# Kernel optimization log

Measured on AMD Instinct MI355X. Metric: run time of the kernel, lower is better.

## Reference

```python
import jax, jax.numpy as jnp
import numpy as np

N_HEAD = 16
THETA = 10000.0


def _rope_cos_sin(T, head_dim):
    # freqs: (T, head_dim//2), matches torch.polar(ones, outer(t, 1/theta^(2i/d)))
    inv = 1.0 / (THETA ** (jnp.arange(0, head_dim, 2, dtype=jnp.float32) / head_dim))
    freqs = jnp.arange(T, dtype=jnp.float32)[:, None] * inv[None, :]
    # broadcast shape (1, T, 1, head_dim//2) over (B, T, H, head_dim//2)
    return jnp.cos(freqs)[None, :, None, :], jnp.sin(freqs)[None, :, None, :]


def _apply_rope(t, cos, sin):
    # t: (B, T, H, hd); pairs (even, odd) form complex numbers
    B, T, H, hd = t.shape
    tr = t.astype(jnp.float32).reshape(B, T, H, hd // 2, 2)
    re, im = tr[..., 0], tr[..., 1]
    out = jnp.stack([re * cos - im * sin, re * sin + im * cos], axis=-1)
    return out.reshape(B, T, H, hd).astype(t.dtype)


def setup_inputs() -> dict:
    key = jax.random.key(0)
    k1, k2, k3 = jax.random.split(key, 3)
    C = 1024
    x = jax.random.normal(k1, (4, 2048, C), dtype=jnp.float32)
    w_attn = jax.random.normal(k2, (3 * C, C), dtype=jnp.float32) * 0.02
    w_proj = jax.random.normal(k3, (C, C), dtype=jnp.float32) * 0.02
    return {"x": x, "w_attn": w_attn, "w_proj": w_proj}


def reference(x, w_attn, w_proj):
    B, T, C = x.shape
    H = N_HEAD
    hd = C // H
    qkv = x @ w_attn.T  # (B, T, 3C) fused QKV projection
    q, k, v = jnp.split(qkv, 3, axis=-1)
    q = q.reshape(B, T, H, hd)
    k = k.reshape(B, T, H, hd)
    v = v.reshape(B, T, H, hd).transpose(0, 2, 1, 3)  # (B, H, T, hd)
    cos, sin = _rope_cos_sin(T, hd)
    q = _apply_rope(q, cos, sin).transpose(0, 2, 1, 3)  # (B, H, T, hd)
    k = _apply_rope(k, cos, sin).transpose(0, 2, 1, 3)
    scale = 1.0 / jnp.sqrt(jnp.float32(hd))
    scores = jnp.einsum('bhqd,bhkd->bhqk', q, k) * scale
    attn = jax.nn.softmax(scores, axis=-1)
    y = jnp.einsum('bhqk,bhkd->bhqd', attn, v)  # (B, H, T, hd)
    y = y.transpose(0, 2, 1, 3).reshape(B, T, C)
    return y @ w_proj.T
```

## Files before the change

### kernel.cpp

```cpp
#include <hip/hip_runtime.h>
#include <math.h>

#define BATCH 4
#define TSEQ 2048
#define CDIM 1024
#define NHEAD 16
#define HDIM 64
#define M_ROWS (BATCH * TSEQ)

typedef float f32x4 __attribute__((ext_vector_type(4)));
typedef __bf16 bf16x8 __attribute__((ext_vector_type(8)));
typedef unsigned int u32x4 __attribute__((ext_vector_type(4)));

typedef const __attribute__((address_space(1))) void gas_void;
typedef __attribute__((address_space(3))) void las_void;

static __device__ __forceinline__ unsigned short f2bf(float f) {
    unsigned int x = __float_as_uint(f);
    x += 0x7fffu + ((x >> 16) & 1u);
    return (unsigned short)(x >> 16);
}

__global__ void prep_kernel(const float* __restrict__ x, unsigned short* __restrict__ xb,
                            const float* __restrict__ wa, unsigned short* __restrict__ wab,
                            const float* __restrict__ wp, unsigned short* __restrict__ wpb,
                            float* __restrict__ cosT, float* __restrict__ sinT) {
    int blk = blockIdx.x;
    if (blk < 6144) {
        const float* in;
        unsigned short* out;
        int base;
        if (blk < 4096)      { in = x;  out = xb;  base = blk; }
        else if (blk < 5632) { in = wa; out = wab; base = blk - 4096; }
        else                 { in = wp; out = wpb; base = blk - 5632; }
        int i = (base * 256 + threadIdx.x) << 3;
        float4 a = *(const float4*)(in + i);
        float4 b = *(const float4*)(in + i + 4);
        union { unsigned short u[8]; u32x4 v; } pk;
        pk.u[0] = f2bf(a.x); pk.u[1] = f2bf(a.y); pk.u[2] = f2bf(a.z); pk.u[3] = f2bf(a.w);
        pk.u[4] = f2bf(b.x); pk.u[5] = f2bf(b.y); pk.u[6] = f2bf(b.z); pk.u[7] = f2bf(b.w);
        *(u32x4*)(out + i) = pk.v;
    } else {
        int idx = (blk - 6144) * 256 + threadIdx.x;
        int t = idx >> 5;
        int i = idx & 31;
        double inv = pow(10000.0, -((double)(2 * i)) / (double)HDIM);
        double ph = (double)t * inv;
        cosT[idx] = (float)cos(ph);
        sinT[idx] = (float)sin(ph);
    }
}

#define GROW(p) (((p) & 64) + (((p) & 15) << 2) + (((p) >> 4) & 3))
#define GEMM_CORE(A_, B_, K_, bm_, bn_)                                          \
    const int tid = threadIdx.x;                                                 \
    const int w = tid >> 6, lane = tid & 63;                                     \
    const int l15 = lane & 15, quad = lane >> 4;                                 \
    const int wm = w >> 1, wn = w & 1;                                           \
    const int ksw = ((lane & 7) ^ ((lane >> 3) & 7)) << 3;                       \
    const int rx = l15 & 7;                                                      \
    const unsigned short* Ag[4]; const unsigned short* Bg[4];                    \
    unsigned short* Al[4]; unsigned short* Bl[4];                                \
    _Pragma("unroll")                                                            \
    for (int i = 0; i < 4; ++i) {                                                \
        const int row = (w << 5) + (i << 3) + (lane >> 3);                       \
        Ag[i] = A_ + (size_t)(bm_ + row) * K_ + ksw;                             \
        Bg[i] = B_ + (size_t)(bn_ + GROW(row)) * K_ + ksw;                       \
        Al[i] = As + row * 64 + ((lane & 7) << 3);                               \
        Bl[i] = Bs + row * 64 + ((lane & 7) << 3);                               \
    }                                                                            \
    f32x4 acc[4][4];                                                             \
    _Pragma("unroll")                                                            \
    for (int i = 0; i < 4; ++i)                                                  \
        _Pragma("unroll")                                                        \
        for (int j = 0; j < 4; ++j) acc[i][j] = (f32x4){0.f, 0.f, 0.f, 0.f};     \
    _Pragma("unroll")                                                            \
    for (int t = 0; t < K_ / 64; ++t) {                                          \
        _Pragma("unroll")                                                        \
        for (int i = 0; i < 4; ++i) {                                            \
            __builtin_amdgcn_global_load_lds((gas_void*)(Ag[i] + t * 64), (las_void*)Al[i], 16, 0, 0); \
            __builtin_amdgcn_global_load_lds((gas_void*)(Bg[i] + t * 64), (las_void*)Bl[i], 16, 0, 0); \
        }                                                                        \
        __syncthreads();                                                         \
        _Pragma("unroll")                                                        \
        for (int kk = 0; kk < 2; ++kk) {                                         \
            bf16x8 af[4], bf[4];                                                 \
            _Pragma("unroll")                                                    \
            for (int mi = 0; mi < 4; ++mi)                                       \
                af[mi] = __builtin_bit_cast(bf16x8,                              \
                    *(const u32x4*)(As + ((wm << 6) + (mi << 4) + l15) * 64 + ((((kk << 2) + quad) ^ rx) << 3))); \
            _Pragma("unroll")                                                    \
            for (int ni = 0; ni < 4; ++ni)                                       \
                bf[ni] = __builtin_bit_cast(bf16x8,                              \
                    *(const u32x4*)(Bs + ((wn << 6) + (ni << 4) + l15) * 64 + ((((kk << 2) + quad) ^ rx) << 3))); \
            _Pragma("unroll")                                                    \
            for (int mi = 0; mi < 4; ++mi)                                       \
                _Pragma("unroll")                                                \
                for (int ni = 0; ni < 4; ++ni)                                   \
                    acc[mi][ni] = __builtin_amdgcn_mfma_f32_16x16x32_bf16(af[mi], bf[ni], acc[mi][ni], 0, 0, 0); \
        }                                                                        \
        __syncthreads();                                                         \
    }

__global__ __launch_bounds__(256) void gemm_qkv_fused(
        const unsigned short* __restrict__ A, const unsigned short* __restrict__ B,
        unsigned short* __restrict__ qb, unsigned short* __restrict__ kb,
        unsigned short* __restrict__ vb,
        const float* __restrict__ cosT, const float* __restrict__ sinT) {
    __shared__ __align__(16) unsigned short As[128 * 64];
    __shared__ __align__(16) unsigned short Bs[128 * 64];
    const int orig = blockIdx.y * 24 + blockIdx.x;
    const int swz  = (orig & 7) * 192 + (orig >> 3);
    const int bm = (swz / 24) << 7;
    const int bn = (swz % 24) << 7;
    GEMM_CORE(A, B, CDIM, bm, bn)

    const int nbase = bn + (wn << 6);
    const int mbase = bm + (wm << 6);
    const int b = mbase >> 11;
    const int tt0 = mbase & (TSEQ - 1);
    const int d0 = l15 << 2;
    const int fi = l15 << 1;

    if (nbase < 2 * CDIM) {
        const int isQ = (nbase < CDIM) ? 1 : 0;
        unsigned short* dst = isQ ? qb : kb;
        const float qs = isQ ? 0.18033688f : 1.0f;
        const int h = (nbase & (CDIM - 1)) >> 6;
        unsigned short* hb = dst + (size_t)(b * NHEAD + h) * TSEQ * HDIM;
#pragma unroll
        for (int mi = 0; mi < 4; ++mi) {
#pragma unroll
            for (int r = 0; r < 4; ++r) {
                const int t = tt0 + (mi << 4) + (quad << 2) + r;
                float2 cc = *(const float2*)(cosT + (t << 5) + fi);
                float2 ss = *(const float2*)(sinT + (t << 5) + fi);
                float re0 = acc[mi][0][r], im0 = acc[mi][1][r];
                float re1 = acc[mi][2][r], im1 = acc[mi][3][r];
                union { unsigned short u[4]; uint2 v; } pk;
                pk.u[0] = f2bf((re0 * cc.x - im0 * ss.x) * qs);
                pk.u[1] = f2bf((re0 * ss.x + im0 * cc.x) * qs);
                pk.u[2] = f2bf((re1 * cc.y - im1 * ss.y) * qs);
                pk.u[3] = f2bf((re1 * ss.y + im1 * cc.y) * qs);
                *(uint2*)(hb + (size_t)t * HDIM + d0) = pk.v;
            }
        }
    } else {
        const int h = (nbase - 2 * CDIM) >> 6;
        unsigned short* hb = vb + (size_t)(b * NHEAD + h) * HDIM * TSEQ;
#pragma unroll
        for (int mi = 0; mi < 4; ++mi) {
            const int t0 = tt0 + (mi << 4) + (quad << 2);
#pragma unroll
            for (int ni = 0; ni < 4; ++ni) {
                const int d = d0 + ni;
                union { unsigned short u[4]; uint2 v; } pk;
#pragma unroll
                for (int r = 0; r < 4; ++r) pk.u[r] = f2bf(acc[mi][ni][r]);
                *(uint2*)(hb + (size_t)d * TSEQ + t0) = pk.v;
            }
        }
    }
}

__global__ __launch_bounds__(256) void gemm_proj(
        const unsigned short* __restrict__ A, const unsigned short* __restrict__ B,
        float* __restrict__ C) {
    __shared__ __align__(16) unsigned short As[128 * 64];
    __shared__ __align__(16) unsigned short Bs[128 * 64];
    const int orig = blockIdx.y * 8 + blockIdx.x;
    const int swz  = (orig & 7) * 64 + (orig >> 3);
    const int bm = (swz >> 3) << 7;
    const int bn = (swz & 7) << 7;
    GEMM_CORE(A, B, CDIM, bm, bn)

#pragma unroll
    for (int mi = 0; mi < 4; ++mi)
#pragma unroll
        for (int r = 0; r < 4; ++r) {
            const int row = bm + (wm << 6) + (mi << 4) + (quad << 2) + r;
            float4 v = make_float4(acc[mi][0][r], acc[mi][1][r], acc[mi][2][r], acc[mi][3][r]);
            *(float4*)(C + (size_t)row * CDIM + bn + (wn << 6) + (l15 << 2)) = v;
        }
}

#define KTILE 64
#define NKT (TSEQ / KTILE)
#define QBLK 256
#define SWZ(row, ch) (((row) << 6) + ((((ch) ^ ((row) & 7))) << 3))
__global__ __launch_bounds__(256, 2) void attn_mfma(
        const unsigned short* __restrict__ qb, const unsigned short* __restrict__ kb,
        const unsigned short* __restrict__ vb, unsigned short* __restrict__ y) {
    const int bh = blockIdx.x;
    const int qt = blockIdx.y;
    const int b = bh >> 4, h = bh & 15;
    const int tid  = threadIdx.x;
    const int w    = tid >> 6;
    const int lane = tid & 63;
    const int l15  = lane & 15;
    const int quad = lane >> 4;

    __shared__ __align__(16) unsigned short Ks[2][KTILE * 64];
    __shared__ __align__(16) unsigned short Vs[2][HDIM * 64];

    const size_t qoff = ((size_t)bh * TSEQ + qt * QBLK + w * 64) * HDIM;
    bf16x8 aq[4][2];
#pragma unroll
    for (int ni = 0; ni < 4; ++ni)
#pragma unroll
        for (int kc = 0; kc < 2; ++kc) {
            u32x4 v = *(const u32x4*)(qb + qoff + (size_t)(ni * 16 + l15) * HDIM + kc * 32 + quad * 8);
            aq[ni][kc] = __builtin_bit_cast(bf16x8, v);
        }

    const u32x4 ones_u = (u32x4){0x3F803F80u, 0x3F803F80u, 0x3F803F80u, 0x3F803F80u};
    const bf16x8 vone = __builtin_bit_cast(bf16x8, ones_u);

    f32x4 o[4][4];
    f32x4 lac[4];
#pragma unroll
    for (int ni = 0; ni < 4; ++ni) {
        lac[ni] = (f32x4){0.f, 0.f, 0.f, 0.f};
#pragma unroll
        for (int nc = 0; nc < 4; ++nc) o[ni][nc] = (f32x4){0.f, 0.f, 0.f, 0.f};
    }

    const unsigned short* kbase = kb + (size_t)bh * TSEQ * HDIM;
    const unsigned short* vbase = vb + (size_t)bh * HDIM * TSEQ;

    const int sr = tid >> 3;
    const int s8 = tid & 7;
    const int sp = s8 << 3;
    const int stK0 = SWZ(sr, s8);
    const int stK1 = SWZ(sr + 32, s8);
    const int fv = (sr & 24) | ((sr & 1) << 2) | ((sr >> 1) & 3);
    const int vrow0 = ((fv & 3) << 4) + (fv >> 2);
    const int vrow1 = vrow0 + 8;
    const int chV  = ((s8 >> 2) << 2) + ((s8 & 1) << 1);
    const int offV = ((s8 >> 1) & 1) << 2;
    const int e0 = vrow0 & 7;
    const int stV00 = (vrow0 << 6) + ((chV ^ e0) << 3) + offV;
    const int stV01 = (vrow0 << 6) + (((chV + 1) ^ e0) << 3) + offV;
    const int stV10 = (vrow1 << 6) + ((chV ^ e0) << 3) + offV;
    const int stV11 = (vrow1 << 6) + (((chV + 1) ^ e0) << 3) + offV;

    u32x4 kr[2], vr[2];
#pragma unroll
    for (int l = 0; l < 2; ++l) {
        kr[l] = *(const u32x4*)(kbase + (size_t)(sr + (l << 5)) * HDIM + sp);
        vr[l] = *(const u32x4*)(vbase + (size_t)(fv + (l << 5)) * TSEQ + sp);
    }
    *(u32x4*)&Ks[0][stK0] = kr[0];
    *(u32x4*)&Ks[0][stK1] = kr[1];
    *(uint2*)&Vs[0][stV00] = make_uint2(vr[0][0], vr[0][1]);
    *(uint2*)&Vs[0][stV01] = make_uint2(vr[0][2], vr[0][3]);
    *(uint2*)&Vs[0][stV10] = make_uint2(vr[1][0], vr[1][1]);
    *(uint2*)&Vs[0][stV11] = make_uint2(vr[1][2], vr[1][3]);
#pragma unroll
    for (int l = 0; l < 2; ++l) {
        kr[l] = *(const u32x4*)(kbase + (size_t)(KTILE + sr + (l << 5)) * HDIM + sp);
        vr[l] = *(const u32x4*)(vbase + (size_t)(fv + (l << 5)) * TSEQ + KTILE + sp);
    }

    for (int kt = 0; kt < NKT; ++kt) {
        const int cur = kt & 1;
        __syncthreads();

        bf16x8 ap[4][2];
#pragma unroll
        for (int pvk = 0; pvk < 2; ++pvk) {
            f32x4 s[2][4];
#pragma unroll
            for (int mi2 = 0; mi2 < 2; ++mi2) {
                const int rowK = (pvk * 2 + mi2) * 16 + l15;
                bf16x8 k0 = __builtin_bit_cast(bf16x8, *(const u32x4*)&Ks[cur][SWZ(rowK, quad)]);
                bf16x8 k1 = __builtin_bit_cast(bf16x8, *(const u32x4*)&Ks[cur][SWZ(rowK, quad ^ 4)]);
#pragma unroll
                for (int ni = 0; ni < 4; ++ni) {
                    f32x4 a2 = (f32x4){0.f, 0.f, 0.f, 0.f};
                    a2 = __builtin_amdgcn_mfma_f32_16x16x32_bf16(k0, aq[ni][0], a2, 0, 0, 0);
                    a2 = __builtin_amdgcn_mfma_f32_16x16x32_bf16(k1, aq[ni][1], a2, 0, 0, 0);
                    s[mi2][ni] = a2;
                }
            }
#pragma unroll
            for (int ni = 0; ni < 4; ++ni) {
                float p0[4], p1[4];
#pragma unroll
                for (int r = 0; r < 4; ++r) {
                    p0[r] = __builtin_amdgcn_exp2f(s[0][ni][r]);
                    p1[r] = __builtin_amdgcn_exp2f(s[1][ni][r]);
                }
                u32x4 pk;
                pk[0] = __builtin_amdgcn_perm(__float_as_uint(p0[1]), __float_as_uint(p0[0]), 0x07060302u);
                pk[1] = __builtin_amdgcn_perm(__float_as_uint(p0[3]), __float_as_uint(p0[2]), 0x07060302u);
                pk[2] = __builtin_amdgcn_perm(__float_as_uint(p1[1]), __float_as_uint(p1[0]), 0x07060302u);
                pk[3] = __builtin_amdgcn_perm(__float_as_uint(p1[3]), __float_as_uint(p1[2]), 0x07060302u);
                ap[ni][pvk] = __builtin_bit_cast(bf16x8, pk);
            }
        }

        if (kt + 1 < NKT) {
            const int nxt = cur ^ 1;
            *(u32x4*)&Ks[nxt][stK0] = kr[0];
            *(u32x4*)&Ks[nxt][stK1] = kr[1];
            *(uint2*)&Vs[nxt][stV00] = make_uint2(vr[0][0], vr[0][1]);
            *(uint2*)&Vs[nxt][stV01] = make_uint2(vr[0][2], vr[0][3]);
            *(uint2*)&Vs[nxt][stV10] = make_uint2(vr[1][0], vr[1][1]);
            *(uint2*)&Vs[nxt][stV11] = make_uint2(vr[1][2], vr[1][3]);
            if (kt + 2 < NKT) {
                int base = (kt + 2) * KTILE;
#pragma unroll
                for (int l = 0; l < 2; ++l) {
                    kr[l] = *(const u32x4*)(kbase + (size_t)(base + sr + (l << 5)) * HDIM + sp);
                    vr[l] = *(const u32x4*)(vbase + (size_t)(fv + (l << 5)) * TSEQ + base + sp);
                }
            }
        }

#pragma unroll
        for (int ni = 0; ni < 4; ++ni) {
            lac[ni] = __builtin_amdgcn_mfma_f32_16x16x32_bf16(ap[ni][0], vone, lac[ni], 0, 0, 0);
            lac[ni] = __builtin_amdgcn_mfma_f32_16x16x32_bf16(ap[ni][1], vone, lac[ni], 0, 0, 0);
        }

#pragma unroll
        for (int nc = 0; nc < 4; ++nc) {
            const int rowV = nc * 16 + l15;
#pragma unroll
            for (int kc = 0; kc < 2; ++kc) {
                bf16x8 bv = __builtin_bit_cast(bf16x8,
                    *(const u32x4*)&Vs[cur][SWZ(rowV, (kc << 2) + quad)]);
#pragma unroll
                for (int ni = 0; ni < 4; ++ni)
                    o[ni][nc] = __builtin_amdgcn_mfma_f32_16x16x32_bf16(ap[ni][kc], bv, o[ni][nc], 0, 0, 0);
            }
        }
    }

#pragma unroll
    for (int ni = 0; ni < 4; ++ni)
#pragma unroll
        for (int r = 0; r < 4; ++r) {
            float inv_l = 1.f / lac[ni][r];
            int t = qt * QBLK + w * 64 + ni * 16 + quad * 4 + r;
            unsigned short* row = y + (size_t)(b * TSEQ + t) * CDIM + h * HDIM;
            union { unsigned short u[4]; uint2 v; } pk;
#pragma unroll
            for (int nc = 0; nc < 4; ++nc) pk.u[nc] = f2bf(o[ni][nc][r] * inv_l);
            *(uint2*)(row + (l15 << 2)) = pk.v;
        }
}

extern "C" void kernel_launch(void* const* d_in, const int* in_sizes, int n_in,
                              void* d_out, int out_size, void* d_ws, size_t ws_size,
                              hipStream_t stream) {
    const float* x      = (const float*)d_in[0];
    const float* w_attn = (const float*)d_in[1];
    const float* w_proj = (const float*)d_in[2];
    float* out = (float*)d_out;

    unsigned short* xb  = (unsigned short*)d_ws;
    unsigned short* wab = xb  + (size_t)M_ROWS * CDIM;
    unsigned short* wpb = wab + (size_t)3 * CDIM * CDIM;
    unsigned short* qb  = wpb + (size_t)CDIM * CDIM;
    unsigned short* kb  = qb  + (size_t)BATCH * NHEAD * TSEQ * HDIM;
    unsigned short* vb  = kb  + (size_t)BATCH * NHEAD * TSEQ * HDIM;
    unsigned short* yb  = vb  + (size_t)BATCH * NHEAD * TSEQ * HDIM;
    float* cosT = (float*)(yb + (size_t)M_ROWS * CDIM);
    float* sinT = cosT + TSEQ * (HDIM / 2);

    prep_kernel<<<6400, 256, 0, stream>>>(x, xb, w_attn, wab, w_proj, wpb, cosT, sinT);

    dim3 g1(3 * CDIM / 128, M_ROWS / 128);
    gemm_qkv_fused<<<g1, 256, 0, stream>>>(xb, wab, qb, kb, vb, cosT, sinT);

    dim3 g2(BATCH * NHEAD, TSEQ / QBLK);
    attn_mfma<<<g2, 256, 0, stream>>>(qb, kb, vb, yb);

    dim3 g3(CDIM / 128, M_ROWS / 128);
    gemm_proj<<<g3, 256, 0, stream>>>(yb, wpb, out);
}
```

Before: 234.2 us.

## Software-pipeline attention loop: overlap PV of previous tile with QK of next

Restructures the attention main loop so each iteration runs the P·V MFMAs for the previous key tile alongside the QK/exp work for the current tile, using two ping-pong probability register sets. The V shared buffer grows from two to four stages because V tiles now live one iteration longer, and the loop is unrolled by four with explicit prologue and epilogue. The aim is to give the scheduler independent MFMA and exp work to interleave and hide latency. The cost is more registers for the second probability set and more LDS, which may threaten two-blocks-per-CU occupancy.

```diff
diff --git a/kernel.cpp b/kernel.cpp
--- a/kernel.cpp
+++ b/kernel.cpp
@@ -188,6 +188,86 @@
 #define NKT (TSEQ / KTILE)
 #define QBLK 256
 #define SWZ(row, ch) (((row) << 6) + ((((ch) ^ ((row) & 7))) << 3))
+
+#define STAGE_KV(KSN, VSN) do {                                                  \
+    *(u32x4*)&Ks[KSN][stK0] = kr[0];                                             \
+    *(u32x4*)&Ks[KSN][stK1] = kr[1];                                             \
+    *(uint2*)&Vs[VSN][stV00] = make_uint2(vr[0][0], vr[0][1]);                   \
+    *(uint2*)&Vs[VSN][stV01] = make_uint2(vr[0][2], vr[0][3]);                   \
+    *(uint2*)&Vs[VSN][stV10] = make_uint2(vr[1][0], vr[1][1]);                   \
+    *(uint2*)&Vs[VSN][stV11] = make_uint2(vr[1][2], vr[1][3]);                   \
+} while (0)
+
+#define LOAD_KV(BASE) do {                                                       \
+    _Pragma("unroll")                                                            \
+    for (int l = 0; l < 2; ++l) {                                                \
+        kr[l] = *(const u32x4*)(kbase + (size_t)((BASE) + sr + (l << 5)) * HDIM + sp); \
+        vr[l] = *(const u32x4*)(vbase + (size_t)(fv + (l << 5)) * TSEQ + (BASE) + sp); \
+    }                                                                            \
+} while (0)
+
+#define QK_SM(KSC, APO) do {                                                     \
+    _Pragma("unroll")                                                            \
+    for (int pvk = 0; pvk < 2; ++pvk) {                                          \
+        f32x4 s[2][4];                                                           \
+        _Pragma("unroll")                                                        \
+        for (int mi2 = 0; mi2 < 2; ++mi2) {                                      \
+            const int rowK = (pvk * 2 + mi2) * 16 + l15;                         \
+            bf16x8 k0 = __builtin_bit_cast(bf16x8, *(const u32x4*)&Ks[KSC][SWZ(rowK, quad)]); \
+            bf16x8 k1 = __builtin_bit_cast(bf16x8, *(const u32x4*)&Ks[KSC][SWZ(rowK, quad ^ 4)]); \
+            _Pragma("unroll")                                                    \
+            for (int ni = 0; ni < 4; ++ni) {                                     \
+                f32x4 a2 = (f32x4){0.f, 0.f, 0.f, 0.f};                          \
+                a2 = __builtin_amdgcn_mfma_f32_16x16x32_bf16(k0, aq[ni][0], a2, 0, 0, 0); \
+                a2 = __builtin_amdgcn_mfma_f32_16x16x32_bf16(k1, aq[ni][1], a2, 0, 0, 0); \
+                s[mi2][ni] = a2;                                                 \
+            }                                                                    \
+        }                                                                        \
+        _Pragma("unroll")                                                        \
+        for (int ni = 0; ni < 4; ++ni) {                                         \
+            float p0[4], p1[4];                                                  \
+            _Pragma("unroll")                                                    \
+            for (int r = 0; r < 4; ++r) {                                        \
+                p0[r] = __builtin_amdgcn_exp2f(s[0][ni][r]);                     \
+                p1[r] = __builtin_amdgcn_exp2f(s[1][ni][r]);                     \
+            }                                                                    \
+            u32x4 pk;                                                            \
+            pk[0] = __builtin_amdgcn_perm(__float_as_uint(p0[1]), __float_as_uint(p0[0]), 0x07060302u); \
+            pk[1] = __builtin_amdgcn_perm(__float_as_uint(p0[3]), __float_as_uint(p0[2]), 0x07060302u); \
+            pk[2] = __builtin_amdgcn_perm(__float_as_uint(p1[1]), __float_as_uint(p1[0]), 0x07060302u); \
+            pk[3] = __builtin_amdgcn_perm(__float_as_uint(p1[3]), __float_as_uint(p1[2]), 0x07060302u); \
+            APO[ni][pvk] = __builtin_bit_cast(bf16x8, pk);                       \
+        }                                                                        \
+    }                                                                            \
+} while (0)
+
+#define PV_L(VSP, API) do {                                                      \
+    _Pragma("unroll")                                                            \
+    for (int ni = 0; ni < 4; ++ni) {                                             \
+        lac[ni] = __builtin_amdgcn_mfma_f32_16x16x32_bf16(API[ni][0], vone, lac[ni], 0, 0, 0); \
+        lac[ni] = __builtin_amdgcn_mfma_f32_16x16x32_bf16(API[ni][1], vone, lac[ni], 0, 0, 0); \
+    }                                                                            \
+    _Pragma("unroll")                                                            \
+    for (int nc = 0; nc < 4; ++nc) {                                             \
+        const int rowV = nc * 16 + l15;                                          \
+        _Pragma("unroll")                                                        \
+        for (int kc = 0; kc < 2; ++kc) {                                         \
+            bf16x8 bv = __builtin_bit_cast(bf16x8, *(const u32x4*)&Vs[VSP][SWZ(rowV, (kc << 2) + quad)]); \
+            _Pragma("unroll")                                                    \
+            for (int ni = 0; ni < 4; ++ni)                                       \
+                o[ni][nc] = __builtin_amdgcn_mfma_f32_16x16x32_bf16(API[ni][kc], bv, o[ni][nc], 0, 0, 0); \
+        }                                                                        \
+    }                                                                            \
+} while (0)
+
+#define ATTN_IT(JV, KSC, VSP, KSN, VSN, API, APO, DOST, DOLD) do {               \
+    __syncthreads();                                                             \
+    PV_L(VSP, API);                                                              \
+    QK_SM(KSC, APO);                                                             \
+    if (DOST) STAGE_KV(KSN, VSN);                                                \
+    if (DOLD) LOAD_KV(((JV) + 2) * KTILE);                                       \
+} while (0)
+
 __global__ __launch_bounds__(256, 2) void attn_mfma(
         const unsigned short* __restrict__ qb, const unsigned short* __restrict__ kb,
         const unsigned short* __restrict__ vb, unsigned short* __restrict__ y) {
@@ -201,7 +281,7 @@
     const int quad = lane >> 4;
 
     __shared__ __align__(16) unsigned short Ks[2][KTILE * 64];
-    __shared__ __align__(16) unsigned short Vs[2][HDIM * 64];
+    __shared__ __align__(16) unsigned short Vs[4][HDIM * 64];
 
     const size_t qoff = ((size_t)bh * TSEQ + qt * QBLK + w * 64) * HDIM;
     bf16x8 aq[4][2];
@@ -244,99 +324,28 @@
     const int stV10 = (vrow1 << 6) + ((chV ^ e0) << 3) + offV;
     const int stV11 = (vrow1 << 6) + (((chV + 1) ^ e0) << 3) + offV;
 
+    bf16x8 apA[4][2], apB[4][2];
     u32x4 kr[2], vr[2];
-#pragma unroll
-    for (int l = 0; l < 2; ++l) {
-        kr[l] = *(const u32x4*)(kbase + (size_t)(sr + (l << 5)) * HDIM + sp);
-        vr[l] = *(const u32x4*)(vbase + (size_t)(fv + (l << 5)) * TSEQ + sp);
-    }
-    *(u32x4*)&Ks[0][stK0] = kr[0];
-    *(u32x4*)&Ks[0][stK1] = kr[1];
-    *(uint2*)&Vs[0][stV00] = make_uint2(vr[0][0], vr[0][1]);
-    *(uint2*)&Vs[0][stV01] = make_uint2(vr[0][2], vr[0][3]);
-    *(uint2*)&Vs[0][stV10] = make_uint2(vr[1][0], vr[1][1]);
-    *(uint2*)&Vs[0][stV11] = make_uint2(vr[1][2], vr[1][3]);
-#pragma unroll
-    for (int l = 0; l < 2; ++l) {
-        kr[l] = *(const u32x4*)(kbase + (size_t)(KTILE + sr + (l << 5)) * HDIM + sp);
-        vr[l] = *(const u32x4*)(vbase + (size_t)(fv + (l << 5)) * TSEQ + KTILE + sp);
-    }
-
-    for (int kt = 0; kt < NKT; ++kt) {
-        const int cur = kt & 1;
-        __syncthreads();
-
-        bf16x8 ap[4][2];
-#pragma unroll
-        for (int pvk = 0; pvk < 2; ++pvk) {
-            f32x4 s[2][4];
-#pragma unroll
-            for (int mi2 = 0; mi2 < 2; ++mi2) {
-                const int rowK = (pvk * 2 + mi2) * 16 + l15;
-                bf16x8 k0 = __builtin_bit_cast(bf16x8, *(const u32x4*)&Ks[cur][SWZ(rowK, quad)]);
-                bf16x8 k1 = __builtin_bit_cast(bf16x8, *(const u32x4*)&Ks[cur][SWZ(rowK, quad ^ 4)]);
-#pragma unroll
-                for (int ni = 0; ni < 4; ++ni) {
-                    f32x4 a2 = (f32x4){0.f, 0.f, 0.f, 0.f};
-                    a2 = __builtin_amdgcn_mfma_f32_16x16x32_bf16(k0, aq[ni][0], a2, 0, 0, 0);
-                    a2 = __builtin_amdgcn_mfma_f32_16x16x32_bf16(k1, aq[ni][1], a2, 0, 0, 0);
-                    s[mi2][ni] = a2;
-                }
-            }
-#pragma unroll
-            for (int ni = 0; ni < 4; ++ni) {
-                float p0[4], p1[4];
-#pragma unroll
-                for (int r = 0; r < 4; ++r) {
-                    p0[r] = __builtin_amdgcn_exp2f(s[0][ni][r]);
-                    p1[r] = __builtin_amdgcn_exp2f(s[1][ni][r]);
-                }
-                u32x4 pk;
-                pk[0] = __builtin_amdgcn_perm(__float_as_uint(p0[1]), __float_as_uint(p0[0]), 0x07060302u);
-                pk[1] = __builtin_amdgcn_perm(__float_as_uint(p0[3]), __float_as_uint(p0[2]), 0x07060302u);
-                pk[2] = __builtin_amdgcn_perm(__float_as_uint(p1[1]), __float_as_uint(p1[0]), 0x07060302u);
-                pk[3] = __builtin_amdgcn_perm(__float_as_uint(p1[3]), __float_as_uint(p1[2]), 0x07060302u);
-                ap[ni][pvk] = __builtin_bit_cast(bf16x8, pk);
-            }
-        }
-
-        if (kt + 1 < NKT) {
-            const int nxt = cur ^ 1;
-            *(u32x4*)&Ks[nxt][stK0] = kr[0];
-            *(u32x4*)&Ks[nxt][stK1] = kr[1];
-            *(uint2*)&Vs[nxt][stV00] = make_uint2(vr[0][0], vr[0][1]);
-            *(uint2*)&Vs[nxt][stV01] = make_uint2(vr[0][2], vr[0][3]);
-            *(uint2*)&Vs[nxt][stV10] = make_uint2(vr[1][0], vr[1][1]);
-            *(uint2*)&Vs[nxt][stV11] = make_uint2(vr[1][2], vr[1][3]);
-            if (kt + 2 < NKT) {
-                int base = (kt + 2) * KTILE;
-#pragma unroll
-                for (int l = 0; l < 2; ++l) {
-                    kr[l] = *(const u32x4*)(kbase + (size_t)(base + sr + (l << 5)) * HDIM + sp);
-                    vr[l] = *(const u32x4*)(vbase + (size_t)(fv + (l << 5)) * TSEQ + base + sp);
-                }
-            }
-        }
-
-#pragma unroll
-        for (int ni = 0; ni < 4; ++ni) {
-            lac[ni] = __builtin_amdgcn_mfma_f32_16x16x32_bf16(ap[ni][0], vone, lac[ni], 0, 0, 0);
-            lac[ni] = __builtin_amdgcn_mfma_f32_16x16x32_bf16(ap[ni][1], vone, lac[ni], 0, 0, 0);
-        }
-
-#pragma unroll
-        for (int nc = 0; nc < 4; ++nc) {
-            const int rowV = nc * 16 + l15;
-#pragma unroll
-            for (int kc = 0; kc < 2; ++kc) {
-                bf16x8 bv = __builtin_bit_cast(bf16x8,
-                    *(const u32x4*)&Vs[cur][SWZ(rowV, (kc << 2) + quad)]);
-#pragma unroll
-                for (int ni = 0; ni < 4; ++ni)
-                    o[ni][nc] = __builtin_amdgcn_mfma_f32_16x16x32_bf16(ap[ni][kc], bv, o[ni][nc], 0, 0, 0);
-            }
-        }
-    }
+
+    LOAD_KV(0);
+    STAGE_KV(0, 0);
+    LOAD_KV(KTILE);
+
+    __syncthreads();
+    QK_SM(0, apA);
+    STAGE_KV(1, 1);
+    LOAD_KV(2 * KTILE);
+
+    for (int kt = 1; kt < 29; kt += 4) {
+        ATTN_IT(kt,     1, 0, 0, 2, apA, apB, true, true);
+        ATTN_IT(kt + 1, 0, 1, 1, 3, apB, apA, true, true);
+        ATTN_IT(kt + 2, 1, 2, 0, 0, apA, apB, true, true);
+        ATTN_IT(kt + 3, 0, 3, 1, 1, apB, apA, true, true);
+    }
+    ATTN_IT(29, 1, 0, 0, 2, apA, apB, true,  true);
+    ATTN_IT(30, 0, 1, 1, 3, apB, apA, true,  false);
+    ATTN_IT(31, 1, 2, 0, 0, apA, apB, false, false);
+    PV_L(3, apB);
 
 #pragma unroll
     for (int ni = 0; ni < 4; ++ni)
```

Measured after the change: 248.0 us. +5.9%, slower.
